# Kernel tuning notes

Hardware: AMD Instinct MI355X
Metric: run time of the kernel (lower is better)

Reference implementation:

```python
import jax, jax.numpy as jnp
import numpy as np

jax.config.update("jax_enable_x64", True)  # hash math uses int64 like torch

N_EMBD = 1024
ORDERS = (2, 3)
NUM_HEADS = 8
NUM_TABLES = len(ORDERS) * NUM_HEADS  # 16
EMBED_DIM = 64
MAX_ORDER = max(ORDERS)  # 3
TABLE_SIZE = 125000
BATCH, STEPS = 8, 2048
VOCAB = 50257


def setup_inputs() -> dict:
    key = jax.random.key(0)
    k1, k2, k3, k4, k5 = jax.random.split(key, 5)
    token_ids = jax.random.randint(k1, (BATCH, STEPS), 0, VOCAB, dtype=jnp.int64)
    # pick_primes(16, 125000) falls through to [table_size + i]
    table_sizes = np.array([TABLE_SIZE + i for i in range(NUM_TABLES)], dtype=np.int64)
    table_offsets = np.concatenate([[0], np.cumsum(table_sizes)[:-1]]).astype(np.int64)
    total = int(table_sizes.sum())
    unified_table = jax.random.normal(k2, (total, EMBED_DIM), dtype=jnp.float32) * 0.02
    # torch zero-inits out_proj; use small random weights so output is non-degenerate
    out_proj_w = jax.random.normal(k3, (N_EMBD, NUM_TABLES * EMBED_DIM), dtype=jnp.float32) * 0.02
    hash_mults = jax.random.randint(k4, (NUM_TABLES, MAX_ORDER), 1, 2 ** 31, dtype=jnp.int64) | 1
    hash_bias = jax.random.randint(k5, (NUM_TABLES,), 0, 2 ** 31, dtype=jnp.int64)
    order_list = [o for o in ORDERS for _ in range(NUM_HEADS)]
    order_mask = np.zeros((MAX_ORDER, NUM_TABLES), dtype=np.int64)
    for ti, o in enumerate(order_list):
        order_mask[:o, ti] = 1
    return {
        "token_ids": token_ids,
        "unified_table": unified_table,
        "out_proj_w": out_proj_w,
        "hash_mults": hash_mults,
        "hash_bias": hash_bias,
        "order_mask": jnp.asarray(order_mask),
        "table_sizes": jnp.asarray(table_sizes),
        "table_offsets": jnp.asarray(table_offsets),
    }


def reference(token_ids, unified_table, out_proj_w, hash_mults, hash_bias,
              order_mask, table_sizes, table_offsets):
    B, S = token_ids.shape
    # shifted[k, b, s] = token_ids[b, s-k] (zero-padded)  -> [K, B, S]
    shifted = jnp.stack([
        token_ids if k == 0 else jnp.pad(token_ids[:, : S - k], ((0, 0), (k, 0)))
        for k in range(MAX_ORDER)
    ])
    # product[k, t, b, s] = mults[t, k] * shifted[k, b, s] * mask[k, t]
    coeff = (hash_mults.T * order_mask)[:, :, None, None]       # [K, T, 1, 1]
    prod = coeff * shifted[:, None, :, :]                        # [K, T, B, S]
    hashed = prod[0]
    for k in range(1, MAX_ORDER):
        hashed = hashed ^ prod[k]
    hashed = (hashed ^ hash_bias[:, None, None]) % table_sizes[:, None, None]
    idx = hashed + table_offsets[:, None, None]                  # [T, B, S]
    emb = unified_table[idx]                                     # [T, B, S, E]
    emb = jnp.transpose(emb, (1, 2, 0, 3)).reshape(B, S, NUM_TABLES * EMBED_DIM)
    return emb @ out_proj_w.T                                    # [B, S, n_embd]
```

## Files before the change

kernel.cpp:

```cpp
#include <hip/hip_runtime.h>
#include <hip/hip_bf16.h>
#include <stdint.h>

#define S_LEN   2048
#define BATCH   8
#define NPOS    (BATCH * S_LEN)
#define NTAB    16
#define EDIM    64
#define KDIM    (NTAB * EDIM)
#define NOUT    1024

typedef float    f32x4_t  __attribute__((ext_vector_type(4)));
typedef __bf16   bf16x8_t __attribute__((ext_vector_type(8)));
typedef unsigned short ushort8_t __attribute__((ext_vector_type(8)));

__device__ __forceinline__ unsigned short f2bf(float f) {
    uint32_t u = __float_as_uint(f);
    u += 0x7fffu + ((u >> 16) & 1u);
    return (unsigned short)(u >> 16);
}

__global__ __launch_bounds__(256) void wconv_kernel(const float* __restrict__ W,
                                                    unsigned short* __restrict__ Wb) {
    int i = blockIdx.x * 256 + threadIdx.x;
    float4 v = ((const float4*)W)[i];
    ushort4 o;
    o.x = f2bf(v.x); o.y = f2bf(v.y); o.z = f2bf(v.z); o.w = f2bf(v.w);
    ((ushort4*)Wb)[i] = o;
}

__global__ __launch_bounds__(256) void hashgather_kernel(const int* __restrict__ tok,
                                                         const int* __restrict__ mults,
                                                         const int* __restrict__ bias,
                                                         const int* __restrict__ omask,
                                                         const int* __restrict__ tsize,
                                                         const int* __restrict__ toff,
                                                         const float* __restrict__ table,
                                                         unsigned short* __restrict__ emb) {
    __shared__ int rows[16][16];
    const int p0 = blockIdx.x * 16;
    {
        const int i = threadIdx.x >> 4;
        const int t = threadIdx.x & 15;
        const int p = p0 + i;
        const int s = p & (S_LEN - 1);
        uint64_t tk0 = (uint32_t)tok[p];
        uint64_t tk1 = (s >= 1) ? (uint64_t)(uint32_t)tok[p - 1] : 0ull;
        uint64_t tk2 = (s >= 2) ? (uint64_t)(uint32_t)tok[p - 2] : 0ull;
        uint64_t m0 = (uint32_t)mults[t * 3 + 0];
        uint64_t m1 = (uint32_t)mults[t * 3 + 1];
        uint64_t m2 = (uint32_t)mults[t * 3 + 2];
        uint64_t k0v = (uint64_t)(uint32_t)omask[0 * NTAB + t];
        uint64_t k1v = (uint64_t)(uint32_t)omask[1 * NTAB + t];
        uint64_t k2v = (uint64_t)(uint32_t)omask[2 * NTAB + t];
        uint64_t h = (m0 * tk0 * k0v) ^ (m1 * tk1 * k1v) ^ (m2 * tk2 * k2v)
                   ^ (uint64_t)(uint32_t)bias[t];
        uint64_t ts = (uint32_t)tsize[t];
        rows[i][t] = (int)(h % ts) + toff[t];
    }
    __syncthreads();

    const int t = threadIdx.x >> 4;
    const int j = threadIdx.x & 15;
    #pragma unroll
    for (int q = 0; q < 16; ++q) {
        const int row = rows[q][t];
        float4 v = *(const float4*)(table + (size_t)row * EDIM + j * 4);
        ushort4 o;
        o.x = f2bf(v.x); o.y = f2bf(v.y); o.z = f2bf(v.z); o.w = f2bf(v.w);
        *(ushort4*)(emb + ((size_t)(p0 + q) * NTAB + t) * EDIM + j * 4) = o;
    }
}

#define TM 128
#define TN 128
#define BK 32

__global__ __launch_bounds__(256, 3) void gemm_kernel(const unsigned short* __restrict__ A,
                                                      const unsigned short* __restrict__ B,
                                                      float* __restrict__ C) {
    __shared__ __align__(16) unsigned short As[2][TM * BK];
    __shared__ __align__(16) unsigned short Bs[2][TN * BK];

    const int blk = blockIdx.x;
    const int bm = blk >> 3;
    const int bn = blk & 7;
    const int tid = threadIdx.x;
    const int wave = tid >> 6;
    const int lane = tid & 63;
    const int wm = wave >> 1;
    const int wn = wave & 1;

    const int rsub  = lane >> 2;
    const int chunk = lane & 3;

    f32x4_t acc[4][4] = {};

    const size_t K = (size_t)KDIM;
    const size_t baseAm = (size_t)(bm * TM);
    const size_t baseBn = (size_t)(bn * TN);

    for (int k0 = 0; k0 < KDIM; k0 += 2 * BK) {
        #pragma unroll
        for (int kh = 0; kh < 2; ++kh) {
            #pragma unroll
            for (int c = 0; c < 2; ++c) {
                const int rrel = c * 64 + wave * 16;
                const int row  = rrel + rsub;
                const unsigned short* gA = A + (baseAm + row) * K + (k0 + kh * BK) + chunk * 8;
                const unsigned short* gB = B + (baseBn + row) * K + (k0 + kh * BK) + chunk * 8;
                unsigned short* lA = &As[kh][rrel * BK];
                unsigned short* lB = &Bs[kh][rrel * BK];
                __builtin_amdgcn_global_load_lds(
                    (__attribute__((address_space(1))) void*)gA,
                    (__attribute__((address_space(3))) void*)lA, 16, 0, 0);
                __builtin_amdgcn_global_load_lds(
                    (__attribute__((address_space(1))) void*)gB,
                    (__attribute__((address_space(3))) void*)lB, 16, 0, 0);
            }
        }
        __syncthreads();

        const int koff = (lane >> 4) * 8;
        const int r16  = lane & 15;
        #pragma unroll
        for (int kh = 0; kh < 2; ++kh) {
            bf16x8_t bfv[4];
            #pragma unroll
            for (int j = 0; j < 4; ++j) {
                ushort8_t rb = *(const ushort8_t*)&Bs[kh][(wn * 64 + j * 16 + r16) * BK + koff];
                bfv[j] = __builtin_bit_cast(bf16x8_t, rb);
            }
            #pragma unroll
            for (int i = 0; i < 4; ++i) {
                ushort8_t ra = *(const ushort8_t*)&As[kh][(wm * 64 + i * 16 + r16) * BK + koff];
                bf16x8_t af = __builtin_bit_cast(bf16x8_t, ra);
                #pragma unroll
                for (int j = 0; j < 4; ++j)
                    acc[i][j] = __builtin_amdgcn_mfma_f32_16x16x32_bf16(af, bfv[j], acc[i][j], 0, 0, 0);
            }
        }
        __syncthreads();
    }

    const int col = lane & 15;
    const int r0  = (lane >> 4) * 4;
    #pragma unroll
    for (int i = 0; i < 4; ++i)
        #pragma unroll
        for (int j = 0; j < 4; ++j)
            #pragma unroll
            for (int r = 0; r < 4; ++r) {
                int m = bm * TM + wm * 64 + i * 16 + r0 + r;
                int n = bn * TN + wn * 64 + j * 16 + col;
                C[(size_t)m * NOUT + n] = acc[i][j][r];
            }
}

extern "C" void kernel_launch(void* const* d_in, const int* in_sizes, int n_in,
                              void* d_out, int out_size, void* d_ws, size_t ws_size,
                              hipStream_t stream) {
    const int*   tok   = (const int*)d_in[0];
    const float* table = (const float*)d_in[1];
    const float* W     = (const float*)d_in[2];
    const int*   mults = (const int*)d_in[3];
    const int*   bias  = (const int*)d_in[4];
    const int*   omask = (const int*)d_in[5];
    const int*   tsize = (const int*)d_in[6];
    const int*   toff  = (const int*)d_in[7];
    float*       out   = (float*)d_out;

    unsigned short* emb = (unsigned short*)d_ws;
    unsigned short* Wb  = (unsigned short*)((char*)d_ws + (size_t)NPOS * KDIM * 2);

    wconv_kernel<<<(NOUT * KDIM / 4) / 256, 256, 0, stream>>>(W, Wb);
    hashgather_kernel<<<NPOS / 16, 256, 0, stream>>>(tok, mults, bias, omask, tsize, toff, table, emb);
    gemm_kernel<<<1024, 256, 0, stream>>>(emb, Wb, out);
}
```

Baseline: 632.9 us.

## Fuse hash-gather into GEMM, streaming table rows into swizzled LDS per table

Merges the hash/gather kernel and the GEMM into one kernel. Each block owns 64 positions and all 1024 output columns. It gathers each table's 64-dim slice as the K-chunk, converts it to bf16 into double-buffered XOR-swizzled LDS, and prefetches the next table's rows. Weights are read directly from global memory into registers rather than staged in LDS. This removes the 32 MB intermediate embedding write and read, but every block re-reads the full 2 MB bf16 weight matrix from global/L2 with no LDS reuse, and there are only 256 blocks.

After: 646.5 us. 2.1% more time.

```diff
diff --git a/kernel.cpp b/kernel.cpp
--- a/kernel.cpp
+++ b/kernel.cpp
@@ -9,10 +9,10 @@
 #define EDIM    64
 #define KDIM    (NTAB * EDIM)
 #define NOUT    1024
+#define BM      64
 
 typedef float    f32x4_t  __attribute__((ext_vector_type(4)));
 typedef __bf16   bf16x8_t __attribute__((ext_vector_type(8)));
-typedef unsigned short ushort8_t __attribute__((ext_vector_type(8)));
 
 __device__ __forceinline__ unsigned short f2bf(float f) {
     uint32_t u = __float_as_uint(f);
@@ -29,132 +29,117 @@
     ((ushort4*)Wb)[i] = o;
 }
 
-__global__ __launch_bounds__(256) void hashgather_kernel(const int* __restrict__ tok,
-                                                         const int* __restrict__ mults,
-                                                         const int* __restrict__ bias,
-                                                         const int* __restrict__ omask,
-                                                         const int* __restrict__ tsize,
-                                                         const int* __restrict__ toff,
-                                                         const float* __restrict__ table,
-                                                         unsigned short* __restrict__ emb) {
-    __shared__ int rows[16][16];
-    const int p0 = blockIdx.x * 16;
-    {
-        const int i = threadIdx.x >> 4;
-        const int t = threadIdx.x & 15;
-        const int p = p0 + i;
-        const int s = p & (S_LEN - 1);
+__global__ __launch_bounds__(512, 2) void fused_kernel(
+        const int*   __restrict__ tok,
+        const int*   __restrict__ mults,
+        const int*   __restrict__ bias,
+        const int*   __restrict__ omask,
+        const int*   __restrict__ tsize,
+        const int*   __restrict__ toff,
+        const float* __restrict__ table,
+        const unsigned short* __restrict__ Wb,
+        float*       __restrict__ C) {
+    __shared__ int rowbuf[BM][NTAB];
+    __shared__ __align__(16) unsigned short As[2][BM * EDIM];
+
+    const int bm   = blockIdx.x;
+    const int tid  = threadIdx.x;
+    const int lane = tid & 63;
+    const int w    = tid >> 6;
+    const int p0   = bm * BM;
+
+    for (int u = tid; u < BM * NTAB; u += 512) {
+        const int i = u >> 4, t = u & 15;
+        const int p = p0 + i, s = p & (S_LEN - 1);
         uint64_t tk0 = (uint32_t)tok[p];
         uint64_t tk1 = (s >= 1) ? (uint64_t)(uint32_t)tok[p - 1] : 0ull;
         uint64_t tk2 = (s >= 2) ? (uint64_t)(uint32_t)tok[p - 2] : 0ull;
         uint64_t m0 = (uint32_t)mults[t * 3 + 0];
         uint64_t m1 = (uint32_t)mults[t * 3 + 1];
         uint64_t m2 = (uint32_t)mults[t * 3 + 2];
-        uint64_t k0v = (uint64_t)(uint32_t)omask[0 * NTAB + t];
-        uint64_t k1v = (uint64_t)(uint32_t)omask[1 * NTAB + t];
-        uint64_t k2v = (uint64_t)(uint32_t)omask[2 * NTAB + t];
+        uint64_t k0v = (uint32_t)omask[0 * NTAB + t];
+        uint64_t k1v = (uint32_t)omask[1 * NTAB + t];
+        uint64_t k2v = (uint32_t)omask[2 * NTAB + t];
         uint64_t h = (m0 * tk0 * k0v) ^ (m1 * tk1 * k1v) ^ (m2 * tk2 * k2v)
                    ^ (uint64_t)(uint32_t)bias[t];
-        uint64_t ts = (uint32_t)tsize[t];
-        rows[i][t] = (int)(h % ts) + toff[t];
+        rowbuf[i][t] = (int)(h % (uint64_t)(uint32_t)tsize[t]) + toff[t];
     }
     __syncthreads();
 
-    const int t = threadIdx.x >> 4;
-    const int j = threadIdx.x & 15;
-    #pragma unroll
-    for (int q = 0; q < 16; ++q) {
-        const int row = rows[q][t];
-        float4 v = *(const float4*)(table + (size_t)row * EDIM + j * 4);
-        ushort4 o;
-        o.x = f2bf(v.x); o.y = f2bf(v.y); o.z = f2bf(v.z); o.w = f2bf(v.w);
-        *(ushort4*)(emb + ((size_t)(p0 + q) * NTAB + t) * EDIM + j * 4) = o;
+    const int ru = tid >> 3;
+    const int cp = tid & 7;
+    const int sw = (ru & 7) << 4;
+
+    float4 g0, g1;
+    {
+        const float4* src = (const float4*)(table + (size_t)rowbuf[ru][0] * EDIM) + cp;
+        g0 = src[0]; g1 = src[8];
     }
-}
+    {
+        ushort4 o0, o1;
+        o0.x = f2bf(g0.x); o0.y = f2bf(g0.y); o0.z = f2bf(g0.z); o0.w = f2bf(g0.w);
+        o1.x = f2bf(g1.x); o1.y = f2bf(g1.y); o1.z = f2bf(g1.z); o1.w = f2bf(g1.w);
+        char* base = (char*)&As[0][0];
+        *(ushort4*)(base + ((ru * 128 + cp * 8) ^ sw))       = o0;
+        *(ushort4*)(base + ((ru * 128 + (cp + 8) * 8) ^ sw)) = o1;
+    }
+    __syncthreads();
 
-#define TM 128
-#define TN 128
-#define BK 32
+    f32x4_t acc[4][8] = {};
+    const int r16 = lane & 15;
+    const int k16 = lane >> 4;
+    int cur = 0;
 
-__global__ __launch_bounds__(256, 3) void gemm_kernel(const unsigned short* __restrict__ A,
-                                                      const unsigned short* __restrict__ B,
-                                                      float* __restrict__ C) {
-    __shared__ __align__(16) unsigned short As[2][TM * BK];
-    __shared__ __align__(16) unsigned short Bs[2][TN * BK];
+    for (int t = 0; t < NTAB; ++t) {
+        float4 n0, n1;
+        if (t + 1 < NTAB) {
+            const float4* src = (const float4*)(table + (size_t)rowbuf[ru][t + 1] * EDIM) + cp;
+            n0 = src[0]; n1 = src[8];
+        }
 
-    const int blk = blockIdx.x;
-    const int bm = blk >> 3;
-    const int bn = blk & 7;
-    const int tid = threadIdx.x;
-    const int wave = tid >> 6;
-    const int lane = tid & 63;
-    const int wm = wave >> 1;
-    const int wn = wave & 1;
+        bf16x8_t af[4][2];
+        #pragma unroll
+        for (int m = 0; m < 4; ++m)
+            #pragma unroll
+            for (int ks = 0; ks < 2; ++ks) {
+                const int row = m * 16 + r16;
+                const int off = (row * 128 + ks * 64 + k16 * 16) ^ ((row & 7) << 4);
+                af[m][ks] = *(const bf16x8_t*)((const char*)&As[cur][0] + off);
+            }
 
-    const int rsub  = lane >> 2;
-    const int chunk = lane & 3;
-
-    f32x4_t acc[4][4] = {};
-
-    const size_t K = (size_t)KDIM;
-    const size_t baseAm = (size_t)(bm * TM);
-    const size_t baseBn = (size_t)(bn * TN);
-
-    for (int k0 = 0; k0 < KDIM; k0 += 2 * BK) {
+        const unsigned short* Bbase = Wb + (size_t)(w * 128) * KDIM + t * 64 + k16 * 8;
         #pragma unroll
-        for (int kh = 0; kh < 2; ++kh) {
+        for (int n = 0; n < 8; ++n) {
+            const unsigned short* bp = Bbase + (size_t)(n * 16 + r16) * KDIM;
+            bf16x8_t b0 = *(const bf16x8_t*)(bp);
+            bf16x8_t b1 = *(const bf16x8_t*)(bp + 32);
             #pragma unroll
-            for (int c = 0; c < 2; ++c) {
-                const int rrel = c * 64 + wave * 16;
-                const int row  = rrel + rsub;
-                const unsigned short* gA = A + (baseAm + row) * K + (k0 + kh * BK) + chunk * 8;
-                const unsigned short* gB = B + (baseBn + row) * K + (k0 + kh * BK) + chunk * 8;
-                unsigned short* lA = &As[kh][rrel * BK];
-                unsigned short* lB = &Bs[kh][rrel * BK];
-                __builtin_amdgcn_global_load_lds(
-                    (__attribute__((address_space(1))) void*)gA,
-                    (__attribute__((address_space(3))) void*)lA, 16, 0, 0);
-                __builtin_amdgcn_global_load_lds(
-                    (__attribute__((address_space(1))) void*)gB,
-                    (__attribute__((address_space(3))) void*)lB, 16, 0, 0);
+            for (int m = 0; m < 4; ++m) {
+                acc[m][n] = __builtin_amdgcn_mfma_f32_16x16x32_bf16(af[m][0], b0, acc[m][n], 0, 0, 0);
+                acc[m][n] = __builtin_amdgcn_mfma_f32_16x16x32_bf16(af[m][1], b1, acc[m][n], 0, 0, 0);
             }
         }
+
         __syncthreads();
-
-        const int koff = (lane >> 4) * 8;
-        const int r16  = lane & 15;
-        #pragma unroll
-        for (int kh = 0; kh < 2; ++kh) {
-            bf16x8_t bfv[4];
-            #pragma unroll
-            for (int j = 0; j < 4; ++j) {
-                ushort8_t rb = *(const ushort8_t*)&Bs[kh][(wn * 64 + j * 16 + r16) * BK + koff];
-                bfv[j] = __builtin_bit_cast(bf16x8_t, rb);
-            }
-            #pragma unroll
-            for (int i = 0; i < 4; ++i) {
-                ushort8_t ra = *(const ushort8_t*)&As[kh][(wm * 64 + i * 16 + r16) * BK + koff];
-                bf16x8_t af = __builtin_bit_cast(bf16x8_t, ra);
-                #pragma unroll
-                for (int j = 0; j < 4; ++j)
-                    acc[i][j] = __builtin_amdgcn_mfma_f32_16x16x32_bf16(af, bfv[j], acc[i][j], 0, 0, 0);
-            }
+        if (t + 1 < NTAB) {
+            ushort4 o0, o1;
+            o0.x = f2bf(n0.x); o0.y = f2bf(n0.y); o0.z = f2bf(n0.z); o0.w = f2bf(n0.w);
+            o1.x = f2bf(n1.x); o1.y = f2bf(n1.y); o1.z = f2bf(n1.z); o1.w = f2bf(n1.w);
+            char* base = (char*)&As[cur ^ 1][0];
+            *(ushort4*)(base + ((ru * 128 + cp * 8) ^ sw))       = o0;
+            *(ushort4*)(base + ((ru * 128 + (cp + 8) * 8) ^ sw)) = o1;
         }
         __syncthreads();
+        cur ^= 1;
     }
 
-    const int col = lane & 15;
-    const int r0  = (lane >> 4) * 4;
     #pragma unroll
-    for (int i = 0; i < 4; ++i)
+    for (int m = 0; m < 4; ++m)
         #pragma unroll
-        for (int j = 0; j < 4; ++j)
+        for (int n = 0; n < 8; ++n)
             #pragma unroll
-            for (int r = 0; r < 4; ++r) {
-                int m = bm * TM + wm * 64 + i * 16 + r0 + r;
-                int n = bn * TN + wn * 64 + j * 16 + col;
-                C[(size_t)m * NOUT + n] = acc[i][j][r];
-            }
+            for (int r = 0; r < 4; ++r)
+                C[(size_t)(p0 + m * 16 + k16 * 4 + r) * NOUT + w * 128 + n * 16 + r16] = acc[m][n][r];
 }
 
 extern "C" void kernel_launch(void* const* d_in, const int* in_sizes, int n_in,
@@ -170,10 +155,9 @@
     const int*   toff  = (const int*)d_in[7];
     float*       out   = (float*)d_out;
 
-    unsigned short* emb = (unsigned short*)d_ws;
-    unsigned short* Wb  = (unsigned short*)((char*)d_ws + (size_t)NPOS * KDIM * 2);
+    unsigned short* Wb = (unsigned short*)d_ws;
 
     wconv_kernel<<<(NOUT * KDIM / 4) / 256, 256, 0, stream>>>(W, Wb);
-    hashgather_kernel<<<NPOS / 16, 256, 0, stream>>>(tok, mults, bias, omask, tsize, toff, table, emb);
-    gemm_kernel<<<1024, 256, 0, stream>>>(emb, Wb, out);
+    fused_kernel<<<NPOS / BM, 512, 0, stream>>>(tok, mults, bias, omask, tsize, toff,
+                                                table, Wb, out);
 }
```
